# Performance work log

Hardware: AMD Instinct MI355X
Metric: run time of the kernel (lower is better)

Reference implementation:

```python
import jax, jax.numpy as jnp
import numpy as np

# 8-neighbor crop offsets in the exact order used by the torch module:
# (rows, cols) slices relative to the full image; center is [1:-1,1:-1]
_OFFSETS = [
    (slice(0, -2), slice(0, -2)),
    (slice(0, -2), slice(1, -1)),
    (slice(0, -2), slice(2, None)),
    (slice(1, -1), slice(0, -2)),
    (slice(2, None), slice(0, -2)),
    (slice(2, None), slice(1, -1)),
    (slice(2, None), slice(2, None)),
    (slice(1, -1), slice(2, None)),
]


def setup_inputs() -> dict:
    key = jax.random.key(0)
    k1, k2, k3 = jax.random.split(key, 3)
    x = jax.random.normal(k1, (32, 3, 256, 256), dtype=jnp.float32)
    w = jax.random.normal(k2, (3, 5, 8), dtype=jnp.float32)   # (in_ch, lbp_ch, 8)
    wl = jax.random.normal(k3, (5, 64), dtype=jnp.float32)    # (lbp_ch, out_ch)
    return {"x": x, "w": w, "wl": wl}


def reference(x, w, wl):
    # x: [n, i, H, W]; center crop [n, i, H-2, W-2]
    c = x[:, :, 1:-1, 1:-1]
    # 8 shifted sign-differences stacked on new axis l -> [n, i, 8, h, w]
    diffs = jnp.stack([jnp.sign(c - x[:, :, r, cc]) for (r, cc) in _OFFSETS], axis=2)
    # per-input-channel LBP mixing: [n,i,8,h,w] x exp(w)[i,m,8] -> [n,i,m,h,w]
    y = jnp.einsum('nilwh,iml->nimwh', diffs, jnp.exp(w))
    # sum over input channels i and project lbp channel m -> out channel o
    y = jnp.einsum('nimwh,mo->nowh', y, wl)
    # residual concat of cropped input, then zero-pad 1 on each spatial side
    out = jnp.concatenate([c, y], axis=1)
    return jnp.pad(out, ((0, 0), (0, 0), (1, 1), (1, 1)))
```

## Files before the change

### kernel.cpp

```cpp
#include <hip/hip_runtime.h>

#define HH 256
#define WW 256
#define HW (HH * WW)

__global__ void prep_kernel(const float* __restrict__ w, const float* __restrict__ wl,
                            float* __restrict__ ws) {
    int t = threadIdx.x;
    if (t < 120) ws[t] = expf(w[t]);
    if (t >= 128 && t < 128 + 320) {
        int idx = t - 128;
        int o = idx / 5, m = idx - o * 5;
        ws[t] = wl[m * 64 + o];
    }
}

__device__ __forceinline__ float sgnf(float d) {
    return (d > 0.0f) ? 1.0f : ((d < 0.0f) ? -1.0f : 0.0f);
}

__global__ __launch_bounds__(256) void lbp_kernel(
    const float* __restrict__ x,
    const float* __restrict__ ws,
    float* __restrict__ out)
{
    const int tid  = threadIdx.x;
    const int bid  = blockIdx.x;
    const int n    = bid >> 6;
    const int q    = bid & 63;
    const int wv   = tid >> 6;
    const int lane = tid & 63;
    const int r    = q * 4 + wv;
    const int cb   = lane * 4;

    float* ob = out + (size_t)n * 67 * HW + (size_t)r * WW + cb;

    if (r == 0 || r == HH - 1) {
        const float4 z = {0.f, 0.f, 0.f, 0.f};
        #pragma unroll
        for (int ch = 0; ch < 67; ++ch)
            *(float4*)(ob + (size_t)ch * HW) = z;
        return;
    }

    const int cl = (cb == 0) ? 0 : cb - 1;
    const int cr = (cb + 4 > WW - 1) ? WW - 1 : cb + 4;

    const float* xb = x + (size_t)n * 3 * HW + (size_t)r * WW;

    float tacc[5][4];
    #pragma unroll
    for (int m = 0; m < 5; ++m)
        #pragma unroll
        for (int j = 0; j < 4; ++j) tacc[m][j] = 0.f;

    #pragma unroll
    for (int i = 0; i < 3; ++i) {
        const float* xr = xb + (size_t)i * HW;

        float4 m4 = *(const float4*)(xr - WW + cb);
        float4 c4 = *(const float4*)(xr + cb);
        float4 p4 = *(const float4*)(xr + WW + cb);

        float rm[6], rc[6], rp[6];
        rm[0] = xr[-WW + cl]; rm[1] = m4.x; rm[2] = m4.y; rm[3] = m4.z; rm[4] = m4.w; rm[5] = xr[-WW + cr];
        rc[0] = xr[cl];       rc[1] = c4.x; rc[2] = c4.y; rc[3] = c4.z; rc[4] = c4.w; rc[5] = xr[cr];
        rp[0] = xr[ WW + cl]; rp[1] = p4.x; rp[2] = p4.y; rp[3] = p4.z; rp[4] = p4.w; rp[5] = xr[ WW + cr];

        float cv[4];
        #pragma unroll
        for (int j = 0; j < 4; ++j) {
            const float ctr = rc[j + 1];
            cv[j] = ctr;
            float s0 = sgnf(ctr - rm[j]);
            float s1 = sgnf(ctr - rm[j + 1]);
            float s2 = sgnf(ctr - rm[j + 2]);
            float s3 = sgnf(ctr - rc[j]);
            float s4 = sgnf(ctr - rp[j]);
            float s5 = sgnf(ctr - rp[j + 1]);
            float s6 = sgnf(ctr - rp[j + 2]);
            float s7 = sgnf(ctr - rc[j + 2]);

            #pragma unroll
            for (int m = 0; m < 5; ++m) {
                const float* Em = ws + i * 40 + m * 8;
                float a = tacc[m][j];
                a = fmaf(s0, Em[0], a);
                a = fmaf(s1, Em[1], a);
                a = fmaf(s2, Em[2], a);
                a = fmaf(s3, Em[3], a);
                a = fmaf(s4, Em[4], a);
                a = fmaf(s5, Em[5], a);
                a = fmaf(s6, Em[6], a);
                a = fmaf(s7, Em[7], a);
                tacc[m][j] = a;
            }
        }

        float4 cc;
        cc.x = (cb + 0 != 0 && cb + 0 != WW - 1) ? cv[0] : 0.f;
        cc.y = cv[1];
        cc.z = cv[2];
        cc.w = (cb + 3 != WW - 1) ? cv[3] : 0.f;
        *(float4*)(ob + (size_t)i * HW) = cc;
    }

    #pragma unroll
    for (int j = 0; j < 4; ++j) {
        const int col = cb + j;
        if (col == 0 || col == WW - 1) {
            #pragma unroll
            for (int m = 0; m < 5; ++m) tacc[m][j] = 0.f;
        }
    }

    const float* wlT = ws + 128;
    float* yb = ob + (size_t)3 * HW;
    #pragma unroll
    for (int o = 0; o < 64; ++o) {
        const float* wo = wlT + o * 5;
        const float w0 = wo[0], w1 = wo[1], w2 = wo[2], w3 = wo[3], w4 = wo[4];
        float4 y;
        y.x = fmaf(tacc[4][0], w4, fmaf(tacc[3][0], w3, fmaf(tacc[2][0], w2, fmaf(tacc[1][0], w1, tacc[0][0] * w0))));
        y.y = fmaf(tacc[4][1], w4, fmaf(tacc[3][1], w3, fmaf(tacc[2][1], w2, fmaf(tacc[1][1], w1, tacc[0][1] * w0))));
        y.z = fmaf(tacc[4][2], w4, fmaf(tacc[3][2], w3, fmaf(tacc[2][2], w2, fmaf(tacc[1][2], w1, tacc[0][2] * w0))));
        y.w = fmaf(tacc[4][3], w4, fmaf(tacc[3][3], w3, fmaf(tacc[2][3], w2, fmaf(tacc[1][3], w1, tacc[0][3] * w0))));
        *(float4*)(yb + (size_t)o * HW) = y;
    }
}

extern "C" void kernel_launch(void* const* d_in, const int* in_sizes, int n_in,
                              void* d_out, int out_size, void* d_ws, size_t ws_size,
                              hipStream_t stream) {
    const float* x  = (const float*)d_in[0];
    const float* w  = (const float*)d_in[1];
    const float* wl = (const float*)d_in[2];
    float* out = (float*)d_out;
    float* ws  = (float*)d_ws;

    prep_kernel<<<1, 512, 0, stream>>>(w, wl, ws);
    lbp_kernel<<<32 * 64, 256, 0, stream>>>(x, ws, out);
}
```

Before: 570.0 us.

## Split LBP into two kernels with an intermediate 5-channel buffer for projection

The fused kernel is split in two. The first kernel computes the 5 LBP channels and writes them, along with the center crop, to a workspace tensor. The second kernel stages tiles of that tensor in shared memory and writes the 64 projected output channels, with each block handling 4 channels across full rows. The aim is to change the write pattern for the 64-channel output, which dominates traffic, so each block streams long contiguous channel planes instead of scattering across 64 planes per row. The cost is an extra round trip of the 5-channel intermediate through global memory, a third launch, and each block re-reading the intermediate for its channel group.

```diff
diff --git a/kernel.cpp b/kernel.cpp
--- a/kernel.cpp
+++ b/kernel.cpp
@@ -4,24 +4,19 @@
 #define WW 256
 #define HW (HH * WW)
 
-__global__ void prep_kernel(const float* __restrict__ w, const float* __restrict__ wl,
-                            float* __restrict__ ws) {
+__global__ void prep_kernel(const float* __restrict__ w, float* __restrict__ E) {
     int t = threadIdx.x;
-    if (t < 120) ws[t] = expf(w[t]);
-    if (t >= 128 && t < 128 + 320) {
-        int idx = t - 128;
-        int o = idx / 5, m = idx - o * 5;
-        ws[t] = wl[m * 64 + o];
-    }
+    if (t < 120) E[t] = expf(w[t]);
 }
 
 __device__ __forceinline__ float sgnf(float d) {
     return (d > 0.0f) ? 1.0f : ((d < 0.0f) ? -1.0f : 0.0f);
 }
 
-__global__ __launch_bounds__(256) void lbp_kernel(
+__global__ __launch_bounds__(256) void lbp_a(
     const float* __restrict__ x,
-    const float* __restrict__ ws,
+    const float* __restrict__ E,
+    float* __restrict__ t,
     float* __restrict__ out)
 {
     const int tid  = threadIdx.x;
@@ -34,18 +29,19 @@
     const int cb   = lane * 4;
 
     float* ob = out + (size_t)n * 67 * HW + (size_t)r * WW + cb;
+    float* tb = t   + (size_t)n * 5  * HW + (size_t)r * WW + cb;
 
     if (r == 0 || r == HH - 1) {
         const float4 z = {0.f, 0.f, 0.f, 0.f};
         #pragma unroll
-        for (int ch = 0; ch < 67; ++ch)
-            *(float4*)(ob + (size_t)ch * HW) = z;
+        for (int ch = 0; ch < 3; ++ch) *(float4*)(ob + (size_t)ch * HW) = z;
+        #pragma unroll
+        for (int m = 0; m < 5; ++m)  *(float4*)(tb + (size_t)m * HW) = z;
         return;
     }
 
     const int cl = (cb == 0) ? 0 : cb - 1;
     const int cr = (cb + 4 > WW - 1) ? WW - 1 : cb + 4;
-
     const float* xb = x + (size_t)n * 3 * HW + (size_t)r * WW;
 
     float tacc[5][4];
@@ -57,7 +53,6 @@
     #pragma unroll
     for (int i = 0; i < 3; ++i) {
         const float* xr = xb + (size_t)i * HW;
-
         float4 m4 = *(const float4*)(xr - WW + cb);
         float4 c4 = *(const float4*)(xr + cb);
         float4 p4 = *(const float4*)(xr + WW + cb);
@@ -83,7 +78,7 @@
 
             #pragma unroll
             for (int m = 0; m < 5; ++m) {
-                const float* Em = ws + i * 40 + m * 8;
+                const float* Em = E + i * 40 + m * 8;
                 float a = tacc[m][j];
                 a = fmaf(s0, Em[0], a);
                 a = fmaf(s1, Em[1], a);
@@ -98,7 +93,7 @@
         }
 
         float4 cc;
-        cc.x = (cb + 0 != 0 && cb + 0 != WW - 1) ? cv[0] : 0.f;
+        cc.x = (cb != 0) ? cv[0] : 0.f;
         cc.y = cv[1];
         cc.z = cv[2];
         cc.w = (cb + 3 != WW - 1) ? cv[3] : 0.f;
@@ -114,18 +109,66 @@
         }
     }
 
-    const float* wlT = ws + 128;
-    float* yb = ob + (size_t)3 * HW;
     #pragma unroll
-    for (int o = 0; o < 64; ++o) {
-        const float* wo = wlT + o * 5;
-        const float w0 = wo[0], w1 = wo[1], w2 = wo[2], w3 = wo[3], w4 = wo[4];
-        float4 y;
-        y.x = fmaf(tacc[4][0], w4, fmaf(tacc[3][0], w3, fmaf(tacc[2][0], w2, fmaf(tacc[1][0], w1, tacc[0][0] * w0))));
-        y.y = fmaf(tacc[4][1], w4, fmaf(tacc[3][1], w3, fmaf(tacc[2][1], w2, fmaf(tacc[1][1], w1, tacc[0][1] * w0))));
-        y.z = fmaf(tacc[4][2], w4, fmaf(tacc[3][2], w3, fmaf(tacc[2][2], w2, fmaf(tacc[1][2], w1, tacc[0][2] * w0))));
-        y.w = fmaf(tacc[4][3], w4, fmaf(tacc[3][3], w3, fmaf(tacc[2][3], w2, fmaf(tacc[1][3], w1, tacc[0][3] * w0))));
-        *(float4*)(yb + (size_t)o * HW) = y;
+    for (int m = 0; m < 5; ++m) {
+        float4 tv = {tacc[m][0], tacc[m][1], tacc[m][2], tacc[m][3]};
+        *(float4*)(tb + (size_t)m * HW) = tv;
+    }
+}
+
+__global__ __launch_bounds__(512) void lbp_b(
+    const float* __restrict__ t,
+    const float* __restrict__ wl,
+    float* __restrict__ out)
+{
+    __shared__ float tl[5 * 16 * 256];
+
+    const int tid  = threadIdx.x;
+    const int bid  = blockIdx.x;
+    const int n    = bid & 31;
+    const int og   = bid >> 5;
+    const int wv   = tid >> 6;
+    const int lane = tid & 63;
+    const int ch   = og * 4 + (wv >> 1);
+    const int rh   = wv & 1;
+
+    const float* tn = t + (size_t)n * 5 * HW;
+    float* ob = out + (size_t)n * 67 * HW + (size_t)(3 + ch) * HW + (size_t)lane * 4;
+
+    const float w0 = wl[0 * 64 + ch];
+    const float w1 = wl[1 * 64 + ch];
+    const float w2 = wl[2 * 64 + ch];
+    const float w3 = wl[3 * 64 + ch];
+    const float w4 = wl[4 * 64 + ch];
+
+    for (int rb = 0; rb < HH; rb += 16) {
+        #pragma unroll
+        for (int k = 0; k < 10; ++k) {
+            const int f = (k * 512 + tid) * 4;
+            const int m = f >> 12;
+            const int within = f & 4095;
+            float4 v = *(const float4*)(tn + (size_t)m * HW + (size_t)rb * WW + within);
+            *(float4*)(&tl[f]) = v;
+        }
+        __syncthreads();
+
+        #pragma unroll
+        for (int rr8 = 0; rr8 < 8; ++rr8) {
+            const int rr = rh * 8 + rr8;
+            const int base = rr * 256 + lane * 4;
+            float4 t0 = *(const float4*)(&tl[0 * 4096 + base]);
+            float4 t1 = *(const float4*)(&tl[1 * 4096 + base]);
+            float4 t2 = *(const float4*)(&tl[2 * 4096 + base]);
+            float4 t3 = *(const float4*)(&tl[3 * 4096 + base]);
+            float4 t4 = *(const float4*)(&tl[4 * 4096 + base]);
+            float4 y;
+            y.x = fmaf(t4.x, w4, fmaf(t3.x, w3, fmaf(t2.x, w2, fmaf(t1.x, w1, t0.x * w0))));
+            y.y = fmaf(t4.y, w4, fmaf(t3.y, w3, fmaf(t2.y, w2, fmaf(t1.y, w1, t0.y * w0))));
+            y.z = fmaf(t4.z, w4, fmaf(t3.z, w3, fmaf(t2.z, w2, fmaf(t1.z, w1, t0.z * w0))));
+            y.w = fmaf(t4.w, w4, fmaf(t3.w, w3, fmaf(t2.w, w2, fmaf(t1.w, w1, t0.w * w0))));
+            *(float4*)(ob + (size_t)(rb + rr) * WW) = y;
+        }
+        __syncthreads();
     }
 }
 
@@ -136,8 +179,10 @@
     const float* w  = (const float*)d_in[1];
     const float* wl = (const float*)d_in[2];
     float* out = (float*)d_out;
-    float* ws  = (float*)d_ws;
+    float* E   = (float*)d_ws;
+    float* t   = (float*)d_ws + 256;
 
-    prep_kernel<<<1, 512, 0, stream>>>(w, wl, ws);
-    lbp_kernel<<<32 * 64, 256, 0, stream>>>(x, ws, out);
+    prep_kernel<<<1, 128, 0, stream>>>(w, E);
+    lbp_a<<<32 * 64, 256, 0, stream>>>(x, E, t, out);
+    lbp_b<<<512, 512, 0, stream>>>(t, wl, out);
 }
```

Measured after the change: 663.6 us. +16.4%, slower.
